# Optimization experiments

Hardware: AMD Instinct MI355X
Metric: run time of the kernel (lower is better)

## Reference

```python
import jax, jax.numpy as jnp
import numpy as np

R_MAX = 5.0
NUM_BASIS = 8
CUTOFF_P = 6
N_LAYERS = 3
C = 64          # hidden_mul / channels of irreps_conv_out (64x0e+64x1o)
Z = 4           # element_number
AVG_DEG = 32.0  # num-neighbor normalization (E/N)
SQRT3 = 1.7320508075688772
SQRT2 = 1.4142135623730951


def _radial_embedding(r):
    # Bessel basis * polynomial cutoff (RadialEdgeEmbedding)
    rs = jnp.maximum(r, 1e-9)
    n = jnp.arange(1, NUM_BASIS + 1, dtype=r.dtype)  # (B,)
    bessel = jnp.sqrt(2.0 / R_MAX) * jnp.sin(n * jnp.pi * rs[:, None] / R_MAX) / rs[:, None]
    x = r / R_MAX
    p = float(CUTOFF_P)
    fc = (1.0
          - (p + 1.0) * (p + 2.0) / 2.0 * x ** CUTOFF_P
          + p * (p + 2.0) * x ** (CUTOFF_P + 1)
          - p * (p + 1.0) / 2.0 * x ** (CUTOFF_P + 2))
    fc = jnp.where(x < 1.0, fc, 0.0)
    return bessel * fc[:, None]  # (E, NUM_BASIS)


def setup_inputs() -> dict:
    key = jax.random.key(0)
    ks = jax.random.split(key, 20)
    N, E, B = 16000, 512000, 16
    atom_type = jax.random.randint(ks[0], (N,), 0, Z)
    # atoms in a 4A box so most edge lengths fall inside r_max=5
    atom_pos = jax.random.uniform(ks[1], (N, 3), dtype=jnp.float32) * 4.0
    edge_src = jax.random.randint(ks[2], (E,), 0, N)
    edge_dst = jax.random.randint(ks[3], (E,), 0, N)
    edge_cell_shift = jnp.zeros((E, 3), jnp.float32)
    cell = jnp.tile(jnp.eye(3, dtype=jnp.float32) * 10.0, (B, 1, 1)) \
        + 0.01 * jax.random.normal(ks[4], (B, 3, 3), jnp.float32)
    image_index = jax.random.randint(ks[5], (N,), 0, B)
    g = lambda k, s, fan: jax.random.normal(k, s, jnp.float32) / np.sqrt(fan)
    return {
        'atom_type': atom_type, 'atom_pos': atom_pos,
        'edge_src': edge_src, 'edge_dst': edge_dst,
        'edge_cell_shift': edge_cell_shift, 'cell': cell, 'image_index': image_index,
        'w_lin_in': g(ks[6], (Z, C), Z),
        'mlp_w1': g(ks[7], (N_LAYERS, NUM_BASIS, 64), NUM_BASIS),
        'mlp_b1': jnp.zeros((N_LAYERS, 64), jnp.float32),
        'mlp_w2': g(ks[8], (N_LAYERS, 64, 5 * C), 64),
        'w_self_s': g(ks[9], (N_LAYERS, C, C), C),
        'w_self_v': g(ks[10], (N_LAYERS, C, C), C),
        'w_gate': g(ks[11], (N_LAYERS, C, C), C),
        'w_lin1': g(ks[12], (C, 16), C),
        'w_lin2': g(ks[13], (16, 1), 16),
    }


def reference(atom_type, atom_pos, edge_src, edge_dst, edge_cell_shift, cell,
              image_index, w_lin_in, mlp_w1, mlp_b1, mlp_w2,
              w_self_s, w_self_v, w_gate, w_lin1, w_lin2):
    N = atom_pos.shape[0]
    # edge vectors with periodic cell shift
    edge_vec = atom_pos[edge_dst] - atom_pos[edge_src]
    edge_vec = edge_vec + jnp.einsum('ni,nij->nj', edge_cell_shift,
                                     cell.reshape(-1, 3, 3)[image_index[edge_src]])
    r = jnp.linalg.norm(edge_vec, axis=1)                      # (E,)
    unit = edge_vec / jnp.maximum(r, 1e-9)[:, None]
    # spherical harmonics lmax=1, component normalization: y0=1 (implicit), y1=sqrt(3)*unit
    y1 = SQRT3 * unit                                           # (E, 3)
    emb = _radial_embedding(r)                                  # (E, NUM_BASIS)

    # one-hot embedding + input linear (one-hot is all 0e -> scalar channels only)
    onehot = jax.nn.one_hot(atom_type, Z, dtype=atom_pos.dtype)
    s = onehot @ w_lin_in                                       # (N, C) l=0 features
    v = jnp.zeros((N, C, 3), atom_pos.dtype)                    # (N, C, 3) l=1 features

    inv_sqrt_deg = 1.0 / np.sqrt(AVG_DEG)
    for L in range(N_LAYERS):
        # radial MLP -> per-edge per-channel tensor-product path weights
        w = jax.nn.silu(emb @ mlp_w1[L] + mlp_b1[L]) @ mlp_w2[L]  # (E, 5C)
        w1, w2, w3, w4, w5 = jnp.split(w, 5, axis=1)              # (E, C) each
        s_src = s[edge_src]                                       # (E, C)
        v_src = v[edge_src]                                       # (E, C, 3)
        vdoty = jnp.einsum('ecx,ex->ec', v_src, y1)
        # CG tensor-product paths (l<=1):
        m_s = w1 * s_src + w2 * vdoty / SQRT3                     # 0x0->0, 1x1->0
        m_v = (w3[:, :, None] * s_src[:, :, None] * y1[:, None, :]      # 0x1->1
               + w4[:, :, None] * v_src                                  # 1x0->1
               + w5[:, :, None] * jnp.cross(v_src, y1[:, None, :]) / SQRT2)  # 1x1->1
        agg_s = jax.ops.segment_sum(m_s, edge_dst, num_segments=N) * inv_sqrt_deg
        agg_v = jax.ops.segment_sum(m_v, edge_dst, num_segments=N) * inv_sqrt_deg
        # gated self-interaction + resnet
        gate = jax.nn.sigmoid(agg_s @ w_gate[L])                  # (N, C)
        s = s + jax.nn.silu(agg_s @ w_self_s[L])
        v = v + jnp.einsum('ncx,cd->ndx', agg_v, w_self_v[L]) * gate[:, :, None]

    # o3.Linear to 16x0e then 1x0e (only scalar channels map to 0e outputs)
    atomic_energy = (s @ w_lin1) @ w_lin2                         # (N, 1)
    atomic_energy = atomic_energy * 1.0                           # atomic_scale
    return atomic_energy
```

## Files before the change

### kernel.cpp

```cpp
#include <hip/hip_runtime.h>
#include <hip/hip_fp16.h>
#include <math.h>

#define NUM_BASIS 8
#define SQRT3 1.7320508075688772f
#define SQRT2 1.4142135623730951f
#define INV_SQRT_DEG 0.17677669529663687f
#define PI_F 3.14159265358979323846f

typedef _Float16 half8 __attribute__((ext_vector_type(8)));
typedef float float4v __attribute__((ext_vector_type(4)));

__device__ __forceinline__ float sigmoidf_(float x) { return 1.0f / (1.0f + __expf(-x)); }
__device__ __forceinline__ float siluf_(float x) { return x * sigmoidf_(x); }

__device__ __forceinline__ void unp2(unsigned u, float& a, float& b) {
    __half2 h = *reinterpret_cast<__half2*>(&u);
    float2 f = __half22float2(h);
    a = f.x; b = f.y;
}
__device__ __forceinline__ unsigned pk2(float a, float b) {
    __half2 h = __floats2half2_rn(a, b);
    return *reinterpret_cast<unsigned*>(&h);
}

__global__ __launch_bounds__(256) void count_deg(
    const int* __restrict__ dst, int* __restrict__ deg, int E)
{
    int base = (blockIdx.x * blockDim.x + threadIdx.x) * 4;
    if (base + 3 < E) {
        int4 d4 = *(const int4*)(dst + base);
        atomicAdd(&deg[d4.x], 1);
        atomicAdd(&deg[d4.y], 1);
        atomicAdd(&deg[d4.z], 1);
        atomicAdd(&deg[d4.w], 1);
    } else {
        for (int e = base; e < E; e++) atomicAdd(&deg[dst[e]], 1);
    }
}

__global__ __launch_bounds__(1024) void scan_deg(
    const int* __restrict__ deg, int* __restrict__ cursor, int N)
{
    __shared__ int wsum[16];
    __shared__ int carry_s, tot_s;
    int tid = threadIdx.x;
    int wid = tid >> 6, lane = tid & 63;
    if (tid == 0) carry_s = 0;
    __syncthreads();
    for (int base = 0; base < N; base += 16384) {
        int i0 = base + tid * 16;
        int v[16];
        int sum = 0;
        #pragma unroll
        for (int k = 0; k < 16; k++) {
            int i = i0 + k;
            v[k] = (i < N) ? deg[i] : 0;
            sum += v[k];
        }
        int incl = sum;
        #pragma unroll
        for (int off = 1; off < 64; off <<= 1) {
            int t = __shfl_up(incl, off);
            if (lane >= off) incl += t;
        }
        if (lane == 63) wsum[wid] = incl;
        __syncthreads();
        if (wid == 0 && lane < 16) {
            int wv = wsum[lane];
            int wincl = wv;
            #pragma unroll
            for (int off = 1; off < 16; off <<= 1) {
                int t = __shfl_up(wincl, off);
                if (lane >= off) wincl += t;
            }
            wsum[lane] = wincl - wv;
            if (lane == 15) tot_s = wincl;
        }
        __syncthreads();
        int carry = carry_s;
        int run = carry + wsum[wid] + incl - sum;
        #pragma unroll
        for (int k = 0; k < 16; k++) {
            int i = i0 + k;
            if (i < N) cursor[i] = run;
            run += v[k];
        }
        __syncthreads();
        if (tid == 0) carry_s = carry + tot_s;
        __syncthreads();
    }
}

__global__ __launch_bounds__(256) void edge_pre_scatter(
    const float* __restrict__ pos, const int* __restrict__ src,
    const int* __restrict__ dst, const float* __restrict__ cs,
    const float* __restrict__ cell, const int* __restrict__ img,
    int* __restrict__ cursor, _Float16* __restrict__ emb,
    uint2* __restrict__ y14, int2* __restrict__ sdp, int E)
{
    int e = blockIdx.x * blockDim.x + threadIdx.x;
    if (e >= E) return;
    int si = src[e], di = dst[e];
    int slot = atomicAdd(&cursor[di], 1);
    sdp[slot] = make_int2(si, di);
    float vx = pos[di*3+0] - pos[si*3+0];
    float vy = pos[di*3+1] - pos[si*3+1];
    float vz = pos[di*3+2] - pos[si*3+2];
    float c0 = cs[(size_t)e*3+0], c1 = cs[(size_t)e*3+1], c2 = cs[(size_t)e*3+2];
    const float* M = cell + (size_t)img[si] * 9;
    vx += c0*M[0] + c1*M[3] + c2*M[6];
    vy += c0*M[1] + c1*M[4] + c2*M[7];
    vz += c0*M[2] + c1*M[5] + c2*M[8];
    float r  = sqrtf(vx*vx + vy*vy + vz*vz);
    float rs = fmaxf(r, 1e-9f);
    float inv = 1.0f / rs;
    uint2 yv;
    yv.x = pk2(SQRT3*vx*inv, SQRT3*vy*inv);
    yv.y = pk2(SQRT3*vz*inv, 0.f);
    y14[slot] = yv;
    float x = r * (1.0f / 5.0f);
    float x2 = x*x, x6 = x2*x2*x2;
    float fc = 1.0f - 28.0f*x6 + 48.0f*x6*x - 21.0f*x6*x2;
    if (x >= 1.0f) fc = 0.0f;
    float pre = sqrtf(2.0f / 5.0f) * inv * fc;
    float t = PI_F * rs * (1.0f / 5.0f);
    half8 ev;
    #pragma unroll
    for (int n = 1; n <= NUM_BASIS; n++)
        ev[n-1] = (_Float16)(pre * __sinf((float)n * t));
    *(half8*)(emb + (size_t)slot*NUM_BASIS) = ev;
}

__global__ __launch_bounds__(256) void prep_weights(
    const float* __restrict__ W2, _Float16* __restrict__ w2f,
    const float* __restrict__ Wg, const float* __restrict__ Ws,
    const float* __restrict__ Wv, _Float16* __restrict__ wgtf,
    const float* __restrict__ Wl1, const float* __restrict__ Wl2,
    float* __restrict__ wl12)
{
    int idx = blockIdx.x * blockDim.x + threadIdx.x;
    if (idx < 64) {
        float a = 0.f;
        #pragma unroll
        for (int j = 0; j < 16; j++) a = fmaf(Wl1[idx*16 + j], Wl2[j], a);
        wl12[idx] = a;
    }
    if (idx < 3 * 20480) {
        int L  = idx / 20480;
        int r  = idx % 20480;
        int cg = r / 5120;
        int r2 = r % 5120;
        int p  = r2 / 1024;
        int r3 = r2 % 1024;
        int kh = r3 / 512;
        int r4 = r3 % 512;
        int lane = r4 / 8;
        int j  = r4 % 8;
        int k = kh*32 + (lane >> 4)*8 + j;
        int n = p*64 + cg*16 + (lane & 15);
        w2f[idx] = (_Float16)W2[(size_t)L*20480 + k*320 + n];
    } else if (idx < 3*20480 + 3*3*4096) {
        int idx2 = idx - 3*20480;
        int L   = idx2 / 12288;
        int rem = idx2 % 12288;
        int mat = rem / 4096;
        int r2  = rem % 4096;
        int cg  = r2 / 1024;
        int r3  = r2 % 1024;
        int kh  = r3 / 512;
        int r4  = r3 % 512;
        int lane = r4 / 8;
        int j   = r4 % 8;
        int k = kh*32 + (lane >> 4)*8 + j;
        int n = cg*16 + (lane & 15);
        const float* src = (mat == 0) ? Wg : (mat == 1) ? Ws : Wv;
        wgtf[idx2] = (_Float16)src[(size_t)L*4096 + k*64 + n];
    }
}

__device__ __forceinline__ void mlp1_afrag(
    const _Float16* __restrict__ emb, const float* __restrict__ W1,
    const float* __restrict__ B1, int eA, int q, half8 afrag[2])
{
    half8 ev = *(const half8*)(emb + (size_t)eA*8);
    float em[8];
    #pragma unroll
    for (int j = 0; j < 8; j++) em[j] = (float)ev[j];
    #pragma unroll
    for (int kh = 0; kh < 2; kh++) {
        int kb = kh*32 + q*8;
        float hv[8];
        float4 b0 = *(const float4*)(B1 + kb);
        float4 b1 = *(const float4*)(B1 + kb + 4);
        hv[0]=b0.x; hv[1]=b0.y; hv[2]=b0.z; hv[3]=b0.w;
        hv[4]=b1.x; hv[5]=b1.y; hv[6]=b1.z; hv[7]=b1.w;
        #pragma unroll
        for (int jj = 0; jj < 8; jj++) {
            float4 wa = *(const float4*)(W1 + jj*64 + kb);
            float4 wb = *(const float4*)(W1 + jj*64 + kb + 4);
            hv[0] = fmaf(em[jj], wa.x, hv[0]);
            hv[1] = fmaf(em[jj], wa.y, hv[1]);
            hv[2] = fmaf(em[jj], wa.z, hv[2]);
            hv[3] = fmaf(em[jj], wa.w, hv[3]);
            hv[4] = fmaf(em[jj], wb.x, hv[4]);
            hv[5] = fmaf(em[jj], wb.y, hv[5]);
            hv[6] = fmaf(em[jj], wb.z, hv[6]);
            hv[7] = fmaf(em[jj], wb.w, hv[7]);
        }
        #pragma unroll
        for (int j = 0; j < 8; j++)
            afrag[kh][j] = (_Float16)siluf_(hv[j]);
    }
}

__global__ __launch_bounds__(256) void edge_msg_mfma_l0(
    const _Float16* __restrict__ emb, const uint2* __restrict__ y14,
    const int2* __restrict__ sdp,
    const int* __restrict__ type, const float* __restrict__ wlin,
    const float* __restrict__ W1, const float* __restrict__ B1,
    const _Float16* __restrict__ w2f,
    float* __restrict__ aggs, float* __restrict__ aggx,
    float* __restrict__ aggy, float* __restrict__ aggz, int E)
{
    __shared__ _Float16 w2s[8192];
    {
        half8* dstv = (half8*)w2s;
        const half8* srcv = (const half8*)w2f;
        #pragma unroll
        for (int k = 0; k < 4; k++) {
            int t  = threadIdx.x + k*256;
            int cg = t >> 8;
            int r  = t & 255;
            int pp = r >> 7;
            int rk = r & 127;
            dstv[t] = srcv[cg*640 + pp*256 + rk];
        }
    }
    __syncthreads();

    int wave  = (blockIdx.x * blockDim.x + threadIdx.x) >> 6;
    int lane  = threadIdx.x & 63;
    int wbase = wave * 16;
    if (wbase >= E) return;
    int q   = lane >> 4;
    int col = lane & 15;

    int eb = wbase + q*4;
    int d[4], tt[4];
    float y1x[4], y1y[4], y1z[4];
    #pragma unroll
    for (int r = 0; r < 4; r++) {
        int2 sv = sdp[eb + r];
        tt[r] = type[sv.x];
        d[r]  = sv.y;
        uint2 yv = y14[eb + r];
        float dummy;
        unp2(yv.x, y1x[r], y1y[r]);
        unp2(yv.y, y1z[r], dummy);
    }

    half8 afrag[2];
    mlp1_afrag(emb, W1, B1, wbase + col, q, afrag);

    int dnq = __shfl_down(d[0], 16);
    int nd3 = (q == 3) ? -1 : dnq;
    int df = d[0], dl = d[3];
    bool U = (df == dl);
    int dlp = __shfl_up(dl, 16);
    bool link = (q > 0) && (dlp == df);

    #pragma unroll
    for (int cg = 0; cg < 4; cg++) {
        float4v a1 = {0,0,0,0}, a3 = {0,0,0,0};
        const _Float16* wbp = w2s + ((size_t)cg*2048) + (size_t)lane*8;
        {
            half8 b10 = *(const half8*)(wbp + 0*512);
            half8 b11 = *(const half8*)(wbp + 1*512);
            half8 b30 = *(const half8*)(wbp + 2*512);
            half8 b31 = *(const half8*)(wbp + 3*512);
            a1 = __builtin_amdgcn_mfma_f32_16x16x32_f16(afrag[0], b10, a1, 0, 0, 0);
            a1 = __builtin_amdgcn_mfma_f32_16x16x32_f16(afrag[1], b11, a1, 0, 0, 0);
            a3 = __builtin_amdgcn_mfma_f32_16x16x32_f16(afrag[0], b30, a3, 0, 0, 0);
            a3 = __builtin_amdgcn_mfma_f32_16x16x32_f16(afrag[1], b31, a3, 0, 0, 0);
        }
        int c = cg*16 + col;

        float ms[4], mx[4], my[4], mz[4];
        #pragma unroll
        for (int r = 0; r < 4; r++) {
            float s = wlin[tt[r]*64 + c];
            float w3s = a3[r] * s;
            ms[r] = a1[r] * s;
            mx[r] = w3s * y1x[r];
            my[r] = w3s * y1y[r];
            mz[r] = w3s * y1z[r];
        }
        #pragma unroll
        for (int r = 1; r < 4; r++) {
            if (d[r] == d[r-1]) {
                ms[r] += ms[r-1]; mx[r] += mx[r-1];
                my[r] += my[r-1]; mz[r] += mz[r-1];
            }
        }
        float Cs = 0.f, Cx = 0.f, Cy = 0.f, Cz = 0.f;
        #pragma unroll
        for (int it = 0; it < 3; it++) {
            float es = ms[3] + (U ? Cs : 0.f);
            float ex = mx[3] + (U ? Cx : 0.f);
            float ey = my[3] + (U ? Cy : 0.f);
            float ez = mz[3] + (U ? Cz : 0.f);
            float ts = __shfl_up(es, 16);
            float tx = __shfl_up(ex, 16);
            float ty = __shfl_up(ey, 16);
            float tz = __shfl_up(ez, 16);
            Cs = link ? ts : 0.f; Cx = link ? tx : 0.f;
            Cy = link ? ty : 0.f; Cz = link ? tz : 0.f;
        }
        bool hr = true;
        #pragma unroll
        for (int r = 0; r < 4; r++) {
            if (r > 0) hr = hr && (d[r] == d[r-1]);
            float fs = ms[r] + (hr ? Cs : 0.f);
            float fx = mx[r] + (hr ? Cx : 0.f);
            float fy = my[r] + (hr ? Cy : 0.f);
            float fz = mz[r] + (hr ? Cz : 0.f);
            int ndx = (r < 3) ? d[r+1] : nd3;
            if (ndx != d[r] && d[r] >= 0) {
                size_t ai = (size_t)d[r]*64 + c;
                atomicAdd(aggs + ai, fs);
                atomicAdd(aggx + ai, fx);
                atomicAdd(aggy + ai, fy);
                atomicAdd(aggz + ai, fz);
            }
        }
    }
}

__global__ __launch_bounds__(256) void edge_msg_mfma(
    const _Float16* __restrict__ emb, const uint2* __restrict__ y14,
    const int2* __restrict__ sdp,
    const uint2* __restrict__ nf,
    const float* __restrict__ W1, const float* __restrict__ B1,
    const _Float16* __restrict__ w2f,
    float* __restrict__ aggs, float* __restrict__ aggx,
    float* __restrict__ aggy, float* __restrict__ aggz, int E)
{
    __shared__ _Float16 w2s[10240];
    int cgh = blockIdx.x & 1;
    {
        half8* dstv = (half8*)w2s;
        const half8* srcv = (const half8*)w2f + (size_t)cgh*1280;
        #pragma unroll
        for (int k = 0; k < 5; k++)
            dstv[threadIdx.x + k*256] = srcv[threadIdx.x + k*256];
    }
    __syncthreads();

    int wave  = ((blockIdx.x >> 1) << 2) + (threadIdx.x >> 6);
    int lane  = threadIdx.x & 63;
    int wbase = wave * 16;
    if (wbase >= E) return;
    int q   = lane >> 4;
    int col = lane & 15;

    int eb = wbase + q*4;
    int d[4], si[4];
    float y1x[4], y1y[4], y1z[4];
    #pragma unroll
    for (int r = 0; r < 4; r++) {
        int2 sv = sdp[eb + r];
        si[r] = sv.x;
        d[r]  = sv.y;
        uint2 yv = y14[eb + r];
        float dummy;
        unp2(yv.x, y1x[r], y1y[r]);
        unp2(yv.y, y1z[r], dummy);
    }

    uint2 pf[4][2];
    #pragma unroll
    for (int r = 0; r < 4; r++) {
        size_t nb = (size_t)si[r] * 64 + cgh*32 + col;
        pf[r][0] = nf[nb];
        pf[r][1] = nf[nb + 16];
    }

    half8 afrag[2];
    mlp1_afrag(emb, W1, B1, wbase + col, q, afrag);

    int dnq = __shfl_down(d[0], 16);
    int nd3 = (q == 3) ? -1 : dnq;
    int df = d[0], dl = d[3];
    bool U = (df == dl);
    int dlp = __shfl_up(dl, 16);
    bool link = (q > 0) && (dlp == df);

    #pragma unroll
    for (int cgl = 0; cgl < 2; cgl++) {
        float4v acc[5];
        #pragma unroll
        for (int p = 0; p < 5; p++) acc[p] = (float4v){0.f, 0.f, 0.f, 0.f};
        const _Float16* wbp = w2s + ((size_t)cgl*5120) + (size_t)lane*8;
        #pragma unroll
        for (int p = 0; p < 5; p++) {
            half8 bf0 = *(const half8*)(wbp + ((size_t)(p*2 + 0))*512);
            half8 bf1 = *(const half8*)(wbp + ((size_t)(p*2 + 1))*512);
            acc[p] = __builtin_amdgcn_mfma_f32_16x16x32_f16(afrag[0], bf0, acc[p], 0, 0, 0);
            acc[p] = __builtin_amdgcn_mfma_f32_16x16x32_f16(afrag[1], bf1, acc[p], 0, 0, 0);
        }
        int c = (cgh*2 + cgl)*16 + col;

        float ms[4], mx[4], my[4], mz[4];
        #pragma unroll
        for (int r = 0; r < 4; r++) {
            float fsx, fvx, fvy, fvz;
            unp2(pf[r][cgl].x, fsx, fvx);
            unp2(pf[r][cgl].y, fvy, fvz);
            float yx = y1x[r], yy = y1y[r], yz = y1z[r];
            float w1 = acc[0][r], w2 = acc[1][r], w3 = acc[2][r];
            float w4 = acc[3][r], w5 = acc[4][r];
            float vdoty = fvx*yx + fvy*yy + fvz*yz;
            ms[r] = w1*fsx + w2*vdoty*(1.0f/SQRT3);
            float cx = fvy*yz - fvz*yy;
            float cy = fvz*yx - fvx*yz;
            float cz = fvx*yy - fvy*yx;
            mx[r] = w3*fsx*yx + w4*fvx + w5*cx*(1.0f/SQRT2);
            my[r] = w3*fsx*yy + w4*fvy + w5*cy*(1.0f/SQRT2);
            mz[r] = w3*fsx*yz + w4*fvz + w5*cz*(1.0f/SQRT2);
        }
        #pragma unroll
        for (int r = 1; r < 4; r++) {
            if (d[r] == d[r-1]) {
                ms[r] += ms[r-1]; mx[r] += mx[r-1];
                my[r] += my[r-1]; mz[r] += mz[r-1];
            }
        }
        float Cs = 0.f, Cx = 0.f, Cy = 0.f, Cz = 0.f;
        #pragma unroll
        for (int it = 0; it < 3; it++) {
            float es = ms[3] + (U ? Cs : 0.f);
            float ex = mx[3] + (U ? Cx : 0.f);
            float ey = my[3] + (U ? Cy : 0.f);
            float ez = mz[3] + (U ? Cz : 0.f);
            float ts = __shfl_up(es, 16);
            float tx = __shfl_up(ex, 16);
            float ty = __shfl_up(ey, 16);
            float tz = __shfl_up(ez, 16);
            Cs = link ? ts : 0.f; Cx = link ? tx : 0.f;
            Cy = link ? ty : 0.f; Cz = link ? tz : 0.f;
        }
        bool hr = true;
        #pragma unroll
        for (int r = 0; r < 4; r++) {
            if (r > 0) hr = hr && (d[r] == d[r-1]);
            float fs = ms[r] + (hr ? Cs : 0.f);
            float fx = mx[r] + (hr ? Cx : 0.f);
            float fy = my[r] + (hr ? Cy : 0.f);
            float fz = mz[r] + (hr ? Cz : 0.f);
            int ndx = (r < 3) ? d[r+1] : nd3;
            if (ndx != d[r] && d[r] >= 0) {
                size_t ai = (size_t)d[r]*64 + c;
                atomicAdd(aggs + ai, fs);
                atomicAdd(aggx + ai, fx);
                atomicAdd(aggy + ai, fy);
                atomicAdd(aggz + ai, fz);
            }
        }
    }
}

__global__ __launch_bounds__(256) void node_update_mfma(
    uint2* __restrict__ nf,
    float* __restrict__ aggs, float* __restrict__ aggx,
    float* __restrict__ aggy, float* __restrict__ aggz,
    const _Float16* __restrict__ wgtf,
    const int* __restrict__ type, const float* __restrict__ wlin,
    const float* __restrict__ wl12,
    float* __restrict__ out, int first, int do_out, int N)
{
    __shared__ _Float16 wgs[12288];
    {
        half8* dstv = (half8*)wgs;
        const half8* srcv = (const half8*)wgtf;
        #pragma unroll
        for (int k = 0; k < 6; k++)
            dstv[threadIdx.x + k*256] = srcv[threadIdx.x + k*256];
    }

    int wave  = (blockIdx.x * blockDim.x + threadIdx.x) >> 6;
    int lane  = threadIdx.x & 63;
    int wbase = wave * 16;
    bool active = wbase < N;
    int q = lane >> 4, col = lane & 15;

    int nodeA = active ? (wbase + col) : 0;
    if (nodeA >= N) nodeA = N - 1;
    size_t nb = (size_t)nodeA * 64 + q * 8;
    half8 af0[2], af1[2], af2[2], af3[2];
    #pragma unroll
    for (int kh = 0; kh < 2; kh++) {
        const float* p0 = aggs + nb + kh*32;
        const float* p1 = aggx + nb + kh*32;
        const float* p2 = aggy + nb + kh*32;
        const float* p3 = aggz + nb + kh*32;
        float4 a0 = *(const float4*)p0, b0 = *(const float4*)(p0+4);
        float4 a1 = *(const float4*)p1, b1 = *(const float4*)(p1+4);
        float4 a2 = *(const float4*)p2, b2 = *(const float4*)(p2+4);
        float4 a3 = *(const float4*)p3, b3 = *(const float4*)(p3+4);
        af0[kh][0]=(_Float16)(a0.x*INV_SQRT_DEG); af0[kh][1]=(_Float16)(a0.y*INV_SQRT_DEG);
        af0[kh][2]=(_Float16)(a0.z*INV_SQRT_DEG); af0[kh][3]=(_Float16)(a0.w*INV_SQRT_DEG);
        af0[kh][4]=(_Float16)(b0.x*INV_SQRT_DEG); af0[kh][5]=(_Float16)(b0.y*INV_SQRT_DEG);
        af0[kh][6]=(_Float16)(b0.z*INV_SQRT_DEG); af0[kh][7]=(_Float16)(b0.w*INV_SQRT_DEG);
        af1[kh][0]=(_Float16)(a1.x*INV_SQRT_DEG); af1[kh][1]=(_Float16)(a1.y*INV_SQRT_DEG);
        af1[kh][2]=(_Float16)(a1.z*INV_SQRT_DEG); af1[kh][3]=(_Float16)(a1.w*INV_SQRT_DEG);
        af1[kh][4]=(_Float16)(b1.x*INV_SQRT_DEG); af1[kh][5]=(_Float16)(b1.y*INV_SQRT_DEG);
        af1[kh][6]=(_Float16)(b1.z*INV_SQRT_DEG); af1[kh][7]=(_Float16)(b1.w*INV_SQRT_DEG);
        af2[kh][0]=(_Float16)(a2.x*INV_SQRT_DEG); af2[kh][1]=(_Float16)(a2.y*INV_SQRT_DEG);
        af2[kh][2]=(_Float16)(a2.z*INV_SQRT_DEG); af2[kh][3]=(_Float16)(a2.w*INV_SQRT_DEG);
        af2[kh][4]=(_Float16)(b2.x*INV_SQRT_DEG); af2[kh][5]=(_Float16)(b2.y*INV_SQRT_DEG);
        af2[kh][6]=(_Float16)(b2.z*INV_SQRT_DEG); af2[kh][7]=(_Float16)(b2.w*INV_SQRT_DEG);
        af3[kh][0]=(_Float16)(a3.x*INV_SQRT_DEG); af3[kh][1]=(_Float16)(a3.y*INV_SQRT_DEG);
        af3[kh][2]=(_Float16)(a3.z*INV_SQRT_DEG); af3[kh][3]=(_Float16)(a3.w*INV_SQRT_DEG);
        af3[kh][4]=(_Float16)(b3.x*INV_SQRT_DEG); af3[kh][5]=(_Float16)(b3.y*INV_SQRT_DEG);
        af3[kh][6]=(_Float16)(b3.z*INV_SQRT_DEG); af3[kh][7]=(_Float16)(b3.w*INV_SQRT_DEG);
    }

    int tt[4];
    #pragma unroll
    for (int r = 0; r < 4; r++) {
        int nd = wbase + q*4 + r;
        tt[r] = type[(active && nd < N) ? nd : 0];
    }

    __syncthreads();

    float epart[4] = {0.f, 0.f, 0.f, 0.f};

    #pragma unroll
    for (int cg = 0; cg < 4; cg++) {
        const _Float16* bp = wgs + (size_t)lane * 8;
        half8 bg0 = *(const half8*)(bp + ((size_t)((0*4 + cg)*2 + 0))*512);
        half8 bg1 = *(const half8*)(bp + ((size_t)((0*4 + cg)*2 + 1))*512);
        half8 bs0 = *(const half8*)(bp + ((size_t)((1*4 + cg)*2 + 0))*512);
        half8 bs1 = *(const half8*)(bp + ((size_t)((1*4 + cg)*2 + 1))*512);
        half8 bv0 = *(const half8*)(bp + ((size_t)((2*4 + cg)*2 + 0))*512);
        half8 bv1 = *(const half8*)(bp + ((size_t)((2*4 + cg)*2 + 1))*512);
        float4v ag = {0,0,0,0}, as = {0,0,0,0};
        float4v ox = {0,0,0,0}, oy = {0,0,0,0}, oz = {0,0,0,0};
        ag = __builtin_amdgcn_mfma_f32_16x16x32_f16(af0[0], bg0, ag, 0, 0, 0);
        ag = __builtin_amdgcn_mfma_f32_16x16x32_f16(af0[1], bg1, ag, 0, 0, 0);
        as = __builtin_amdgcn_mfma_f32_16x16x32_f16(af0[0], bs0, as, 0, 0, 0);
        as = __builtin_amdgcn_mfma_f32_16x16x32_f16(af0[1], bs1, as, 0, 0, 0);
        ox = __builtin_amdgcn_mfma_f32_16x16x32_f16(af1[0], bv0, ox, 0, 0, 0);
        ox = __builtin_amdgcn_mfma_f32_16x16x32_f16(af1[1], bv1, ox, 0, 0, 0);
        oy = __builtin_amdgcn_mfma_f32_16x16x32_f16(af2[0], bv0, oy, 0, 0, 0);
        oy = __builtin_amdgcn_mfma_f32_16x16x32_f16(af2[1], bv1, oy, 0, 0, 0);
        oz = __builtin_amdgcn_mfma_f32_16x16x32_f16(af3[0], bv0, oz, 0, 0, 0);
        oz = __builtin_amdgcn_mfma_f32_16x16x32_f16(af3[1], bv1, oz, 0, 0, 0);

        if (!active) continue;
        int c = cg*16 + col;
        float wlc = wl12[c];
        #pragma unroll
        for (int r = 0; r < 4; r++) {
            int nd = wbase + q*4 + r;
            bool wr = nd < N;
            size_t ni = (size_t)nd*64 + c;
            float sx, vx, vy, vz;
            if (first) {
                sx = wlin[tt[r]*64 + c];
                vx = 0.f; vy = 0.f; vz = 0.f;
            } else {
                uint2 cur = nf[wr ? ni : 0];
                unp2(cur.x, sx, vx);
                unp2(cur.y, vy, vz);
            }
            float gate = sigmoidf_(ag[r]);
            sx += siluf_(as[r]);
            vx += ox[r] * gate;
            vy += oy[r] * gate;
            vz += oz[r] * gate;
            if (wr) {
                uint2 nv;
                nv.x = pk2(sx, vx);
                nv.y = pk2(vy, vz);
                nf[ni] = nv;
                aggs[ni] = 0.f;
                aggx[ni] = 0.f;
                aggy[ni] = 0.f;
                aggz[ni] = 0.f;
                epart[r] = fmaf(sx, wlc, epart[r]);
            }
        }
    }
    if (do_out && active) {
        #pragma unroll
        for (int r = 0; r < 4; r++) {
            float e = epart[r];
            e += __shfl_xor(e, 1);
            e += __shfl_xor(e, 2);
            e += __shfl_xor(e, 4);
            e += __shfl_xor(e, 8);
            int nd = wbase + q*4 + r;
            if (col == 0 && nd < N) out[nd] = e;
        }
    }
}

extern "C" void kernel_launch(void* const* d_in, const int* in_sizes, int n_in,
                              void* d_out, int out_size, void* d_ws, size_t ws_size,
                              hipStream_t stream)
{
    const int*   atom_type = (const int*)  d_in[0];
    const float* pos       = (const float*)d_in[1];
    const int*   src       = (const int*)  d_in[2];
    const int*   dst       = (const int*)  d_in[3];
    const float* cs        = (const float*)d_in[4];
    const float* cell      = (const float*)d_in[5];
    const int*   img       = (const int*)  d_in[6];
    const float* wlin_in   = (const float*)d_in[7];
    const float* mw1       = (const float*)d_in[8];
    const float* mb1       = (const float*)d_in[9];
    const float* mw2       = (const float*)d_in[10];
    const float* wss       = (const float*)d_in[11];
    const float* wsv       = (const float*)d_in[12];
    const float* wg        = (const float*)d_in[13];
    const float* wl1       = (const float*)d_in[14];
    const float* wl2       = (const float*)d_in[15];
    int N = in_sizes[0];
    int E = in_sizes[2];

    char* w = (char*)d_ws;
    _Float16* emb = (_Float16*)w; w += (size_t)E * 8 * sizeof(_Float16);
    uint2*  y14  = (uint2*)w;  w += (size_t)E * sizeof(uint2);
    int2*   sdp  = (int2*)w;   w += (size_t)E * sizeof(int2);
    uint2*  nf   = (uint2*)w;  w += (size_t)N * 64 * sizeof(uint2);
    float*  agg  = (float*)w;  w += (size_t)N * 64 * 4 * sizeof(float);
    _Float16* w2f  = (_Float16*)w; w += (size_t)3 * 20480 * sizeof(_Float16);
    _Float16* wgtf = (_Float16*)w; w += (size_t)3 * 3 * 4096 * sizeof(_Float16);
    float*  wl12 = (float*)w;  w += 64 * sizeof(float);
    int*    deg  = (int*)w;    w += (size_t)N * sizeof(int);
    int*    curs = (int*)w;    w += (size_t)N * sizeof(int);

    size_t NC = (size_t)N * 64;
    float* aggs = agg;
    float* aggx = agg + NC;
    float* aggy = agg + 2*NC;
    float* aggz = agg + 3*NC;

    hipMemsetAsync(deg, 0, (size_t)N * sizeof(int), stream);
    hipMemsetAsync(agg, 0, NC * 4 * sizeof(float), stream);
    count_deg<<<(E/4 + 255) / 256, 256, 0, stream>>>(dst, deg, E);
    scan_deg<<<1, 1024, 0, stream>>>(deg, curs, N);
    int prep_n = 3*20480 + 3*3*4096;
    prep_weights<<<(prep_n + 255) / 256, 256, 0, stream>>>(
        mw2, w2f, wg, wss, wsv, wgtf, wl1, wl2, wl12);
    edge_pre_scatter<<<(E + 255) / 256, 256, 0, stream>>>(
        pos, src, dst, cs, cell, img, curs, emb, y14, sdp, E);

    int eblocks = (E + 63) / 64;
    int nblocks = (N + 63) / 64;

    edge_msg_mfma_l0<<<eblocks, 256, 0, stream>>>(
        emb, y14, sdp, atom_type, wlin_in,
        mw1, mb1, w2f, aggs, aggx, aggy, aggz, E);
    node_update_mfma<<<nblocks, 256, 0, stream>>>(
        nf, aggs, aggx, aggy, aggz, wgtf, atom_type, wlin_in, wl12,
        (float*)d_out, 1, 0, N);

    for (int L = 1; L < 3; L++) {
        edge_msg_mfma<<<eblocks * 2, 256, 0, stream>>>(
            emb, y14, sdp, nf,
            mw1 + L * 8 * 64, mb1 + L * 64, w2f + (size_t)L * 20480,
            aggs, aggx, aggy, aggz, E);
        node_update_mfma<<<nblocks, 256, 0, stream>>>(
            nf, aggs, aggx, aggy, aggz,
            wgtf + (size_t)L * 12288, atom_type, wlin_in, wl12,
            (float*)d_out, 0, (L == 2) ? 1 : 0, N);
    }
}
```

Baseline: 523.2 us.

## Process both channel halves per block in edge message kernel, fold CG constants into weights

Result: faster. 461.0 us (-11.9%).

```diff
diff --git a/kernel.cpp b/kernel.cpp
--- a/kernel.cpp
+++ b/kernel.cpp
@@ -159,7 +159,10 @@
         int j  = r4 % 8;
         int k = kh*32 + (lane >> 4)*8 + j;
         int n = p*64 + cg*16 + (lane & 15);
-        w2f[idx] = (_Float16)W2[(size_t)L*20480 + k*320 + n];
+        float val = W2[(size_t)L*20480 + k*320 + n];
+        if (p == 1)      val *= 0.5773502691896258f;
+        else if (p == 4) val *= 0.7071067811865476f;
+        w2f[idx] = (_Float16)val;
     } else if (idx < 3*20480 + 3*3*4096) {
         int idx2 = idx - 3*20480;
         int L   = idx2 / 12288;
@@ -337,65 +340,15 @@
     }
 }
 
-__global__ __launch_bounds__(256) void edge_msg_mfma(
-    const _Float16* __restrict__ emb, const uint2* __restrict__ y14,
-    const int2* __restrict__ sdp,
-    const uint2* __restrict__ nf,
-    const float* __restrict__ W1, const float* __restrict__ B1,
-    const _Float16* __restrict__ w2f,
+__device__ __forceinline__ void process_half(
+    const _Float16* __restrict__ w2s, const half8 afrag[2],
+    const uint2 pf[4][2], const int d[4], int nd3, bool U, bool link,
+    bool live, const float* y1x, const float* y1y, const float* y1z,
+    int cgh, int col,
     float* __restrict__ aggs, float* __restrict__ aggx,
-    float* __restrict__ aggy, float* __restrict__ aggz, int E)
-{
-    __shared__ _Float16 w2s[10240];
-    int cgh = blockIdx.x & 1;
-    {
-        half8* dstv = (half8*)w2s;
-        const half8* srcv = (const half8*)w2f + (size_t)cgh*1280;
-        #pragma unroll
-        for (int k = 0; k < 5; k++)
-            dstv[threadIdx.x + k*256] = srcv[threadIdx.x + k*256];
-    }
-    __syncthreads();
-
-    int wave  = ((blockIdx.x >> 1) << 2) + (threadIdx.x >> 6);
-    int lane  = threadIdx.x & 63;
-    int wbase = wave * 16;
-    if (wbase >= E) return;
-    int q   = lane >> 4;
-    int col = lane & 15;
-
-    int eb = wbase + q*4;
-    int d[4], si[4];
-    float y1x[4], y1y[4], y1z[4];
-    #pragma unroll
-    for (int r = 0; r < 4; r++) {
-        int2 sv = sdp[eb + r];
-        si[r] = sv.x;
-        d[r]  = sv.y;
-        uint2 yv = y14[eb + r];
-        float dummy;
-        unp2(yv.x, y1x[r], y1y[r]);
-        unp2(yv.y, y1z[r], dummy);
-    }
-
-    uint2 pf[4][2];
-    #pragma unroll
-    for (int r = 0; r < 4; r++) {
-        size_t nb = (size_t)si[r] * 64 + cgh*32 + col;
-        pf[r][0] = nf[nb];
-        pf[r][1] = nf[nb + 16];
-    }
-
-    half8 afrag[2];
-    mlp1_afrag(emb, W1, B1, wbase + col, q, afrag);
-
-    int dnq = __shfl_down(d[0], 16);
-    int nd3 = (q == 3) ? -1 : dnq;
-    int df = d[0], dl = d[3];
-    bool U = (df == dl);
-    int dlp = __shfl_up(dl, 16);
-    bool link = (q > 0) && (dlp == df);
-
+    float* __restrict__ aggy, float* __restrict__ aggz)
+{
+    int lane = threadIdx.x & 63;
     #pragma unroll
     for (int cgl = 0; cgl < 2; cgl++) {
         float4v acc[5];
@@ -421,13 +374,14 @@
             float w1 = acc[0][r], w2 = acc[1][r], w3 = acc[2][r];
             float w4 = acc[3][r], w5 = acc[4][r];
             float vdoty = fvx*yx + fvy*yy + fvz*yz;
-            ms[r] = w1*fsx + w2*vdoty*(1.0f/SQRT3);
+            ms[r] = fmaf(w1, fsx, w2*vdoty);
+            float w3s = w3*fsx;
             float cx = fvy*yz - fvz*yy;
             float cy = fvz*yx - fvx*yz;
             float cz = fvx*yy - fvy*yx;
-            mx[r] = w3*fsx*yx + w4*fvx + w5*cx*(1.0f/SQRT2);
-            my[r] = w3*fsx*yy + w4*fvy + w5*cy*(1.0f/SQRT2);
-            mz[r] = w3*fsx*yz + w4*fvz + w5*cz*(1.0f/SQRT2);
+            mx[r] = fmaf(w3s, yx, fmaf(w4, fvx, w5*cx));
+            my[r] = fmaf(w3s, yy, fmaf(w4, fvy, w5*cy));
+            mz[r] = fmaf(w3s, yz, fmaf(w4, fvz, w5*cz));
         }
         #pragma unroll
         for (int r = 1; r < 4; r++) {
@@ -459,7 +413,7 @@
             float fy = my[r] + (hr ? Cy : 0.f);
             float fz = mz[r] + (hr ? Cz : 0.f);
             int ndx = (r < 3) ? d[r+1] : nd3;
-            if (ndx != d[r] && d[r] >= 0) {
+            if (ndx != d[r] && d[r] >= 0 && live) {
                 size_t ai = (size_t)d[r]*64 + c;
                 atomicAdd(aggs + ai, fs);
                 atomicAdd(aggx + ai, fx);
@@ -468,6 +422,95 @@
             }
         }
     }
+}
+
+__global__ __launch_bounds__(256) void edge_msg_mfma(
+    const _Float16* __restrict__ emb, const uint2* __restrict__ y14,
+    const int2* __restrict__ sdp,
+    const uint2* __restrict__ nf,
+    const float* __restrict__ W1, const float* __restrict__ B1,
+    const _Float16* __restrict__ w2f,
+    float* __restrict__ aggs, float* __restrict__ aggx,
+    float* __restrict__ aggy, float* __restrict__ aggz, int E)
+{
+    __shared__ _Float16 w2s[10240];
+    {
+        half8* dstv = (half8*)w2s;
+        const half8* srcv = (const half8*)w2f;
+        #pragma unroll
+        for (int k = 0; k < 5; k++)
+            dstv[threadIdx.x + k*256] = srcv[threadIdx.x + k*256];
+    }
+    __syncthreads();
+
+    int wave  = (blockIdx.x * blockDim.x + threadIdx.x) >> 6;
+    int lane  = threadIdx.x & 63;
+    int wbase = wave * 16;
+    bool live = wbase < E;
+    int wb2   = live ? wbase : 0;
+    int q   = lane >> 4;
+    int col = lane & 15;
+
+    int eb = wb2 + q*4;
+    int d[4], si[4];
+    float y1x[4], y1y[4], y1z[4];
+    #pragma unroll
+    for (int r = 0; r < 4; r++) {
+        int2 sv = sdp[eb + r];
+        si[r] = sv.x;
+        d[r]  = sv.y;
+        uint2 yv = y14[eb + r];
+        float dummy;
+        unp2(yv.x, y1x[r], y1y[r]);
+        unp2(yv.y, y1z[r], dummy);
+    }
+
+    uint2 pf[4][2];
+    #pragma unroll
+    for (int r = 0; r < 4; r++) {
+        size_t nb = (size_t)si[r] * 64 + col;
+        pf[r][0] = nf[nb];
+        pf[r][1] = nf[nb + 16];
+    }
+
+    half8 afrag[2];
+    mlp1_afrag(emb, W1, B1, wb2 + col, q, afrag);
+
+    int dnq = __shfl_down(d[0], 16);
+    int nd3 = (q == 3) ? -1 : dnq;
+    int df = d[0], dl = d[3];
+    bool U = (df == dl);
+    int dlp = __shfl_up(dl, 16);
+    bool link = (q > 0) && (dlp == df);
+
+    process_half(w2s, afrag, pf, d, nd3, U, link, live,
+                 y1x, y1y, y1z, 0, col, aggs, aggx, aggy, aggz);
+
+    #pragma unroll
+    for (int r = 0; r < 4; r++) {
+        size_t nb = (size_t)si[r] * 64 + 32 + col;
+        pf[r][0] = nf[nb];
+        pf[r][1] = nf[nb + 16];
+    }
+
+    asm volatile("s_waitcnt lgkmcnt(0)" ::: "memory");
+    __builtin_amdgcn_s_barrier();
+    asm volatile("" ::: "memory");
+
+    {
+        half8* dstv = (half8*)w2s;
+        const half8* srcv = (const half8*)w2f + 1280;
+        #pragma unroll
+        for (int k = 0; k < 5; k++)
+            dstv[threadIdx.x + k*256] = srcv[threadIdx.x + k*256];
+    }
+
+    asm volatile("s_waitcnt lgkmcnt(0)" ::: "memory");
+    __builtin_amdgcn_s_barrier();
+    asm volatile("" ::: "memory");
+
+    process_half(w2s, afrag, pf, d, nd3, U, link, live,
+                 y1x, y1y, y1z, 1, col, aggs, aggx, aggy, aggz);
 }
 
 __global__ __launch_bounds__(256) void node_update_mfma(
@@ -670,7 +713,7 @@
         (float*)d_out, 1, 0, N);
 
     for (int L = 1; L < 3; L++) {
-        edge_msg_mfma<<<eblocks * 2, 256, 0, stream>>>(
+        edge_msg_mfma<<<eblocks, 256, 0, stream>>>(
             emb, y14, sdp, nf,
             mw1 + L * 8 * 64, mb1 + L * 64, w2f + (size_t)L * 20480,
             aggs, aggx, aggy, aggz, E);
```
